# Performance work log

Hardware: AMD Instinct MI355X
Metric: run time of the kernel (lower is better)

The kernel has to match this reference:

```python
import jax, jax.numpy as jnp
import numpy as np

EPS = 1e-10

def norm_t(x, axis):
    # zero-mean + L2 normalize along `axis` (standard NCC normalization)
    xc = x - jnp.mean(x, axis=axis, keepdims=True)
    return xc / (jnp.linalg.norm(xc, axis=axis, keepdims=True) + EPS)

def setup_inputs() -> dict:
    key = jax.random.key(0)
    k1, k2 = jax.random.split(key)
    input_compressed = jax.random.normal(k1, (1, 16, 131072), dtype=jnp.float32)  # [B, K, N]
    cmat = jax.random.normal(k2, (16, 1024), dtype=jnp.float32)                   # [K, D]
    return {"input_compressed": input_compressed, "cmat": cmat}

def reference(input_compressed, cmat):
    a = norm_t(input_compressed, axis=-2)          # [B, K, N], normalized over K
    b = norm_t(cmat, axis=0)                       # [K, D],    normalized over K
    ncc = jnp.einsum('bkn,kd->bnd', a, b)          # [B, N, D] correlation volume
    # torch: argmax(transpose(ncc,-2,-1), dim=-2) -> argmax over D -> [B, N]
    pred_depths = jnp.argmax(ncc, axis=-1)         # [B, N] int depth-bin indices
    return pred_depths
```

## Files before the change

### kernel.cpp

```cpp
#include <hip/hip_runtime.h>
#include <hip/hip_bf16.h>
#include <math.h>

#define N_PTS  131072
#define K_DIM  16
#define D_BINS 1024
#define MARGIN_P 6e-4f

typedef short bf16x8 __attribute__((ext_vector_type(8)));
typedef float f32x4  __attribute__((ext_vector_type(4)));

#define WS_OFF_BN  64
#define WS_OFF_B1  65600
#define WS_OFF_B2  98368
#define WS_OFF_WL  131152
#define WS_NEED    655440

__device__ __forceinline__ void norm_np(const float* __restrict__ p,
                                        int stride, int n, float* __restrict__ a) {
#pragma clang fp contract(off)
    float v[K_DIM];
#pragma unroll
    for (int k = 0; k < K_DIM; ++k) v[k] = p[(size_t)k * stride + n];
    float s = v[0];
#pragma unroll
    for (int k = 1; k < K_DIM; ++k) s = s + v[k];
    const float mean = s / 16.0f;
    float sq[K_DIM];
#pragma unroll
    for (int k = 0; k < K_DIM; ++k) { a[k] = v[k] - mean; sq[k] = a[k] * a[k]; }
    float ss = sq[0];
#pragma unroll
    for (int k = 1; k < K_DIM; ++k) ss = ss + sq[k];
    const float denom = sqrtf(ss) + 1e-10f;
#pragma unroll
    for (int k = 0; k < K_DIM; ++k) a[k] = a[k] / denom;
}

__device__ __forceinline__ unsigned short bf16_bits(float f) {
    __hip_bfloat16 h = __float2bfloat16(f);
    unsigned short u;
    __builtin_memcpy(&u, &h, 2);
    return u;
}
__device__ __forceinline__ float bf16_val(float f) {
    return __bfloat162float(__float2bfloat16(f));
}

__device__ __forceinline__ unsigned v_med3u(unsigned a, unsigned b, unsigned c) {
    unsigned d;
    asm("v_med3_u32 %0, %1, %2, %3" : "=v"(d) : "v"(a), "v"(b), "v"(c));
    return d;
}

__global__ __launch_bounds__(256) void prep_b(
    const float* __restrict__ cmat, float* __restrict__ bnT,
    unsigned short* __restrict__ B1, unsigned short* __restrict__ B2,
    int* __restrict__ wl_count) {
#pragma clang fp contract(off)
    if (blockIdx.x == 0 && threadIdx.x == 0) *wl_count = 0;
    const int d = blockIdx.x * 256 + threadIdx.x;
    if (d >= D_BINS) return;

    float t[K_DIM];
    norm_np(cmat, D_BINS, d, t);

    const int tile = d >> 4, n = d & 15;
#pragma unroll
    for (int k = 0; k < K_DIM; ++k) {
        bnT[d * K_DIM + k] = t[k];
        const float hi_f = bf16_val(t[k]);
        const int idx = tile * 256 + ((k >> 3) * 16 + n) * 8 + (k & 7);
        B1[idx] = bf16_bits(t[k]);
        B2[idx] = bf16_bits(t[k] - hi_f);
    }
}

__global__ __launch_bounds__(512, 4) void mfma_screen(
    const float* __restrict__ x, const uint4* __restrict__ Bfrag,
    int* __restrict__ out, int* __restrict__ wl, int* __restrict__ wl_count) {
#pragma clang fp contract(off)
    __shared__ uint4 ldsB[4096];

    {
#pragma unroll
        for (int j = 0; j < 8; ++j)
            ldsB[threadIdx.x + j * 512] = Bfrag[threadIdx.x + j * 512];
    }

    const int lane = threadIdx.x & 63;
    const int wv   = threadIdx.x >> 6;
    const int W    = blockIdx.x * 8 + wv;
    const int P    = W * 16;
    const int m    = lane & 15;
    const int q    = lane >> 4;

    bf16x8 A, A2;
    {
        float a[K_DIM];
        norm_np(x, N_PTS, P + m, a);
        unsigned short els[8];
#pragma unroll
        for (int j = 0; j < 8; ++j) {
            const int k = (q & 1) * 8 + j;
            if (q < 2) els[j] = bf16_bits(a[k]);
            else       els[j] = bf16_bits(a[k] - bf16_val(a[k]));
        }
        __builtin_memcpy(&A, els, 16);
        A2 = (q < 2) ? A : (bf16x8)(short)0;
    }

    __syncthreads();

    const uint4* b1p = ldsB + (lane & 31);
    const uint4* b2p = ldsB + 2048 + (lane & 31);

    unsigned ub1[4], ub2[4];
#pragma unroll
    for (int r = 0; r < 4; ++r) { ub1[r] = 0u; ub2[r] = 0u; }

    const unsigned mask  = 0xFFFFF800u;
    const unsigned dbase = 2047u - (unsigned)m;

#pragma unroll 4
    for (int i = 0; i < 64; ++i) {
        const uint4 w1 = b1p[i * 32];
        const uint4 w2 = b2p[i * 32];
        const bf16x8 bf1 = __builtin_bit_cast(bf16x8, w1);
        const bf16x8 bf2 = __builtin_bit_cast(bf16x8, w2);

        f32x4 acc = __builtin_amdgcn_mfma_f32_16x16x32_bf16(
            A, bf1, (f32x4){2.f, 2.f, 2.f, 2.f}, 0, 0, 0);
        acc = __builtin_amdgcn_mfma_f32_16x16x32_bf16(A2, bf2, acc, 0, 0, 0);

        const unsigned dcomp = dbase - (unsigned)(i * 16);
#pragma unroll
        for (int r = 0; r < 4; ++r) {
            const unsigned u   = (__float_as_uint(acc[r]) & mask) | dcomp;
            const unsigned nb2 = v_med3u(ub1[r], ub2[r], u);
            ub1[r] = max(ub1[r], u);
            ub2[r] = nb2;
        }
    }

#pragma unroll
    for (int r = 0; r < 4; ++r) {
        unsigned u1 = ub1[r], u2 = ub2[r];
#pragma unroll
        for (int s = 1; s <= 8; s <<= 1) {
            const unsigned o1 = (unsigned)__shfl_xor((int)u1, s, 16);
            const unsigned o2 = (unsigned)__shfl_xor((int)u2, s, 16);
            const unsigned n1 = max(u1, o1);
            u2 = max(min(u1, o1), max(u2, o2));
            u1 = n1;
        }
        if (m == 0) {
            const int p  = P + q * 4 + r;
            const float s1 = __uint_as_float(u1 & mask);
            const float s2 = __uint_as_float(u2 & mask);
            if (s1 - s2 > MARGIN_P) {
                out[p] = 2047 - (int)(u1 & 2047u);
            } else {
                const int pos = atomicAdd(wl_count, 1);
                wl[pos] = p;
            }
        }
    }
}

__global__ __launch_bounds__(256) void ncc_exact_refine(
    const float* __restrict__ x, const float* __restrict__ bnT,
    int* __restrict__ out, const int* __restrict__ wl,
    const int* __restrict__ wl_count) {
#pragma clang fp contract(off)
    const int count  = *wl_count;
    const int lane   = threadIdx.x & 63;
    const int wave   = (blockIdx.x * 256 + threadIdx.x) >> 6;
    const int nwaves = (gridDim.x * 256) >> 6;

    for (int i = wave; i < count; i += nwaves) {
        const int n = wl[i];
        float a[K_DIM];
        norm_np(x, N_PTS, n, a);

        float best = -3.402823466e38f;
        int   idx  = 0x7fffffff;
        const float4* b4 = (const float4*)bnT;
        for (int t = 0; t < 16; ++t) {
            const int d = t * 64 + lane;
            const float4 q0 = b4[d * 4 + 0];
            const float4 q1 = b4[d * 4 + 1];
            const float4 q2 = b4[d * 4 + 2];
            const float4 q3 = b4[d * 4 + 3];
            float sc;
            sc = a[0] * q0.x;
            sc = sc + a[1]  * q0.y; sc = sc + a[2]  * q0.z; sc = sc + a[3]  * q0.w;
            sc = sc + a[4]  * q1.x; sc = sc + a[5]  * q1.y; sc = sc + a[6]  * q1.z;
            sc = sc + a[7]  * q1.w; sc = sc + a[8]  * q2.x; sc = sc + a[9]  * q2.y;
            sc = sc + a[10] * q2.z; sc = sc + a[11] * q2.w; sc = sc + a[12] * q3.x;
            sc = sc + a[13] * q3.y; sc = sc + a[14] * q3.z; sc = sc + a[15] * q3.w;
            if (sc > best) { best = sc; idx = d; }
        }
#pragma unroll
        for (int mk = 1; mk <= 32; mk <<= 1) {
            const float ob = __shfl_xor(best, mk);
            const int   oi = __shfl_xor(idx,  mk);
            if (ob > best || (ob == best && oi < idx)) { best = ob; idx = oi; }
        }
        if (lane == 0) out[n] = idx;
    }
}

__global__ __launch_bounds__(256) void ncc_argmax_np32(
    const float* __restrict__ x, const float* __restrict__ bnT,
    int* __restrict__ out) {
#pragma clang fp contract(off)
    const int n = blockIdx.x * 256 + threadIdx.x;
    float a[K_DIM];
    norm_np(x, N_PTS, n, a);

    float best = -3.402823466e38f;
    int   idx  = 0;
    const float4* b4 = (const float4*)bnT;
#pragma unroll 2
    for (int d = 0; d < D_BINS; ++d) {
        const float4 q0 = b4[d * 4 + 0];
        const float4 q1 = b4[d * 4 + 1];
        const float4 q2 = b4[d * 4 + 2];
        const float4 q3 = b4[d * 4 + 3];
        float sc;
        sc = a[0] * q0.x;
        sc = sc + a[1]  * q0.y; sc = sc + a[2]  * q0.z; sc = sc + a[3]  * q0.w;
        sc = sc + a[4]  * q1.x; sc = sc + a[5]  * q1.y; sc = sc + a[6]  * q1.z;
        sc = sc + a[7]  * q1.w; sc = sc + a[8]  * q2.x; sc = sc + a[9]  * q2.y;
        sc = sc + a[10] * q2.z; sc = sc + a[11] * q2.w; sc = sc + a[12] * q3.x;
        sc = sc + a[13] * q3.y; sc = sc + a[14] * q3.z; sc = sc + a[15] * q3.w;
        if (sc > best) { best = sc; idx = d; }
    }
    out[n] = idx;
}

__global__ __launch_bounds__(256) void normalize_rows_only(
    const float* __restrict__ cmat, float* __restrict__ bnT) {
#pragma clang fp contract(off)
    const int d = blockIdx.x * 256 + threadIdx.x;
    if (d >= D_BINS) return;
    float t[K_DIM];
    norm_np(cmat, D_BINS, d, t);
#pragma unroll
    for (int k = 0; k < K_DIM; ++k) bnT[d * K_DIM + k] = t[k];
}

extern "C" void kernel_launch(void* const* d_in, const int* in_sizes, int n_in,
                              void* d_out, int out_size, void* d_ws, size_t ws_size,
                              hipStream_t stream) {
    const float* x    = (const float*)d_in[0];
    const float* cmat = (const float*)d_in[1];
    int* out = (int*)d_out;
    char* ws = (char*)d_ws;

    if (ws_size >= (size_t)WS_NEED) {
        int*            wl_count = (int*)ws;
        float*          bnT      = (float*)(ws + WS_OFF_BN);
        unsigned short* B1       = (unsigned short*)(ws + WS_OFF_B1);
        unsigned short* B2       = (unsigned short*)(ws + WS_OFF_B2);
        int*            wl       = (int*)(ws + WS_OFF_WL);

        prep_b<<<4, 256, 0, stream>>>(cmat, bnT, B1, B2, wl_count);
        mfma_screen<<<1024, 512, 0, stream>>>(
            x, (const uint4*)(ws + WS_OFF_B1), out, wl, wl_count);
        ncc_exact_refine<<<512, 256, 0, stream>>>(x, bnT, out, wl, wl_count);
    } else {
        float* bnT = (float*)(ws + WS_OFF_BN);
        normalize_rows_only<<<4, 256, 0, stream>>>(cmat, bnT);
        ncc_argmax_np32<<<512, 256, 0, stream>>>(x, bnT, out);
    }
}
```

Measured before the change: 103.9 us.

## Switch screening MFMA to 32x32x16 tiles with three-term split-bf16 product

The screening kernel now uses 32x32x16 bf16 MFMA so each wave processes 32 points against 32 depth bins per step, and the B fragment layout in prep_b is rebuilt to match. The split-precision product changes from two half-empty 16x16 MFMAs (with a zeroed A2 half) to three full MFMAs (hi*hi, lo*hi, hi*lo), which drops the zero-padding waste. The grid is halved to match 32 points per wave. Each thread now holds 16 accumulators plus 32 running top-2 registers, which raises register pressure and may lower occupancy.

```diff
diff --git a/kernel.cpp b/kernel.cpp
--- a/kernel.cpp
+++ b/kernel.cpp
@@ -9,6 +9,7 @@
 
 typedef short bf16x8 __attribute__((ext_vector_type(8)));
 typedef float f32x4  __attribute__((ext_vector_type(4)));
+typedef float f32x16 __attribute__((ext_vector_type(16)));
 
 #define WS_OFF_BN  64
 #define WS_OFF_B1  65600
@@ -65,12 +66,12 @@
     float t[K_DIM];
     norm_np(cmat, D_BINS, d, t);
 
-    const int tile = d >> 4, n = d & 15;
+    const int tile = d >> 5, col = d & 31;
 #pragma unroll
     for (int k = 0; k < K_DIM; ++k) {
         bnT[d * K_DIM + k] = t[k];
         const float hi_f = bf16_val(t[k]);
-        const int idx = tile * 256 + ((k >> 3) * 16 + n) * 8 + (k & 7);
+        const int idx = tile * 512 + (k >> 3) * 256 + col * 8 + (k & 7);
         B1[idx] = bf16_bits(t[k]);
         B2[idx] = bf16_bits(t[k] - hi_f);
     }
@@ -91,51 +92,55 @@
     const int lane = threadIdx.x & 63;
     const int wv   = threadIdx.x >> 6;
     const int W    = blockIdx.x * 8 + wv;
-    const int P    = W * 16;
-    const int m    = lane & 15;
-    const int q    = lane >> 4;
-
-    bf16x8 A, A2;
+    const int P    = W * 32;
+    const int col  = lane & 31;
+    const int kh   = (lane >> 5) << 3;
+
+    bf16x8 Ahi, Alo;
     {
         float a[K_DIM];
-        norm_np(x, N_PTS, P + m, a);
-        unsigned short els[8];
+        norm_np(x, N_PTS, P + col, a);
+        unsigned short h[8], l[8];
 #pragma unroll
         for (int j = 0; j < 8; ++j) {
-            const int k = (q & 1) * 8 + j;
-            if (q < 2) els[j] = bf16_bits(a[k]);
-            else       els[j] = bf16_bits(a[k] - bf16_val(a[k]));
-        }
-        __builtin_memcpy(&A, els, 16);
-        A2 = (q < 2) ? A : (bf16x8)(short)0;
+            const float v = a[kh + j];
+            h[j] = bf16_bits(v);
+            l[j] = bf16_bits(v - bf16_val(v));
+        }
+        __builtin_memcpy(&Ahi, h, 16);
+        __builtin_memcpy(&Alo, l, 16);
     }
 
     __syncthreads();
 
-    const uint4* b1p = ldsB + (lane & 31);
-    const uint4* b2p = ldsB + 2048 + (lane & 31);
-
-    unsigned ub1[4], ub2[4];
-#pragma unroll
-    for (int r = 0; r < 4; ++r) { ub1[r] = 0u; ub2[r] = 0u; }
+    const uint4* b1p = ldsB + lane;
+    const uint4* b2p = ldsB + 2048 + lane;
+
+    f32x16 cb;
+#pragma unroll
+    for (int r = 0; r < 16; ++r) cb[r] = 2.0f;
+
+    unsigned ub1[16], ub2[16];
+#pragma unroll
+    for (int r = 0; r < 16; ++r) { ub1[r] = 0u; ub2[r] = 0u; }
 
     const unsigned mask  = 0xFFFFF800u;
-    const unsigned dbase = 2047u - (unsigned)m;
+    const unsigned dbase = 2047u - (unsigned)col;
 
 #pragma unroll 4
-    for (int i = 0; i < 64; ++i) {
-        const uint4 w1 = b1p[i * 32];
-        const uint4 w2 = b2p[i * 32];
+    for (int t = 0; t < 32; ++t) {
+        const uint4 w1 = b1p[t * 64];
+        const uint4 w2 = b2p[t * 64];
         const bf16x8 bf1 = __builtin_bit_cast(bf16x8, w1);
         const bf16x8 bf2 = __builtin_bit_cast(bf16x8, w2);
 
-        f32x4 acc = __builtin_amdgcn_mfma_f32_16x16x32_bf16(
-            A, bf1, (f32x4){2.f, 2.f, 2.f, 2.f}, 0, 0, 0);
-        acc = __builtin_amdgcn_mfma_f32_16x16x32_bf16(A2, bf2, acc, 0, 0, 0);
-
-        const unsigned dcomp = dbase - (unsigned)(i * 16);
-#pragma unroll
-        for (int r = 0; r < 4; ++r) {
+        f32x16 acc = __builtin_amdgcn_mfma_f32_32x32x16_bf16(Ahi, bf1, cb, 0, 0, 0);
+        acc = __builtin_amdgcn_mfma_f32_32x32x16_bf16(Alo, bf1, acc, 0, 0, 0);
+        acc = __builtin_amdgcn_mfma_f32_32x32x16_bf16(Ahi, bf2, acc, 0, 0, 0);
+
+        const unsigned dcomp = dbase - (unsigned)(t * 32);
+#pragma unroll
+        for (int r = 0; r < 16; ++r) {
             const unsigned u   = (__float_as_uint(acc[r]) & mask) | dcomp;
             const unsigned nb2 = v_med3u(ub1[r], ub2[r], u);
             ub1[r] = max(ub1[r], u);
@@ -144,18 +149,18 @@
     }
 
 #pragma unroll
-    for (int r = 0; r < 4; ++r) {
+    for (int r = 0; r < 16; ++r) {
         unsigned u1 = ub1[r], u2 = ub2[r];
 #pragma unroll
-        for (int s = 1; s <= 8; s <<= 1) {
-            const unsigned o1 = (unsigned)__shfl_xor((int)u1, s, 16);
-            const unsigned o2 = (unsigned)__shfl_xor((int)u2, s, 16);
+        for (int s = 1; s <= 16; s <<= 1) {
+            const unsigned o1 = (unsigned)__shfl_xor((int)u1, s, 32);
+            const unsigned o2 = (unsigned)__shfl_xor((int)u2, s, 32);
             const unsigned n1 = max(u1, o1);
             u2 = max(min(u1, o1), max(u2, o2));
             u1 = n1;
         }
-        if (m == 0) {
-            const int p  = P + q * 4 + r;
+        if (col == 0) {
+            const int p  = P + (r & 3) + 8 * (r >> 2) + 4 * (lane >> 5);
             const float s1 = __uint_as_float(u1 & mask);
             const float s2 = __uint_as_float(u2 & mask);
             if (s1 - s2 > MARGIN_P) {
@@ -267,7 +272,7 @@
         int*            wl       = (int*)(ws + WS_OFF_WL);
 
         prep_b<<<4, 256, 0, stream>>>(cmat, bnT, B1, B2, wl_count);
-        mfma_screen<<<1024, 512, 0, stream>>>(
+        mfma_screen<<<512, 512, 0, stream>>>(
             x, (const uint4*)(ws + WS_OFF_B1), out, wl, wl_count);
         ncc_exact_refine<<<512, 256, 0, stream>>>(x, bnT, out, wl, wl_count);
     } else {
```

New measurement: 106.5 us. 2.5% more time.

## Fuse exact refinement into MFMA screen kernel, drop global worklist and atomics

Applied to the files above, without the earlier changes.

Ambiguous points whose top-two margin is too small are no longer pushed to a global worklist with atomics for a third kernel. Each wave now collects its failing points into a ballot-built bitmask and refines them exactly in place against the fp32 normalized table. This removes one kernel launch, the atomic counter, and the worklist traffic. The cost is load imbalance, since waves that happen to hold many ambiguous points stall their block while the rest finish.

```diff
diff --git a/kernel.cpp b/kernel.cpp
--- a/kernel.cpp
+++ b/kernel.cpp
@@ -13,8 +13,7 @@
 #define WS_OFF_BN  64
 #define WS_OFF_B1  65600
 #define WS_OFF_B2  98368
-#define WS_OFF_WL  131152
-#define WS_NEED    655440
+#define WS_NEED    131136
 
 __device__ __forceinline__ void norm_np(const float* __restrict__ p,
                                         int stride, int n, float* __restrict__ a) {
@@ -55,10 +54,8 @@
 
 __global__ __launch_bounds__(256) void prep_b(
     const float* __restrict__ cmat, float* __restrict__ bnT,
-    unsigned short* __restrict__ B1, unsigned short* __restrict__ B2,
-    int* __restrict__ wl_count) {
-#pragma clang fp contract(off)
-    if (blockIdx.x == 0 && threadIdx.x == 0) *wl_count = 0;
+    unsigned short* __restrict__ B1, unsigned short* __restrict__ B2) {
+#pragma clang fp contract(off)
     const int d = blockIdx.x * 256 + threadIdx.x;
     if (d >= D_BINS) return;
 
@@ -78,7 +75,7 @@
 
 __global__ __launch_bounds__(512, 4) void mfma_screen(
     const float* __restrict__ x, const uint4* __restrict__ Bfrag,
-    int* __restrict__ out, int* __restrict__ wl, int* __restrict__ wl_count) {
+    const float* __restrict__ bnT, int* __restrict__ out) {
 #pragma clang fp contract(off)
     __shared__ uint4 ldsB[4096];
 
@@ -143,6 +140,7 @@
         }
     }
 
+    unsigned fail16 = 0;
 #pragma unroll
     for (int r = 0; r < 4; ++r) {
         unsigned u1 = ub1[r], u2 = ub2[r];
@@ -154,34 +152,28 @@
             u2 = max(min(u1, o1), max(u2, o2));
             u1 = n1;
         }
+        int fail = 0;
         if (m == 0) {
             const int p  = P + q * 4 + r;
             const float s1 = __uint_as_float(u1 & mask);
             const float s2 = __uint_as_float(u2 & mask);
-            if (s1 - s2 > MARGIN_P) {
-                out[p] = 2047 - (int)(u1 & 2047u);
-            } else {
-                const int pos = atomicAdd(wl_count, 1);
-                wl[pos] = p;
-            }
-        }
-    }
-}
-
-__global__ __launch_bounds__(256) void ncc_exact_refine(
-    const float* __restrict__ x, const float* __restrict__ bnT,
-    int* __restrict__ out, const int* __restrict__ wl,
-    const int* __restrict__ wl_count) {
-#pragma clang fp contract(off)
-    const int count  = *wl_count;
-    const int lane   = threadIdx.x & 63;
-    const int wave   = (blockIdx.x * 256 + threadIdx.x) >> 6;
-    const int nwaves = (gridDim.x * 256) >> 6;
-
-    for (int i = wave; i < count; i += nwaves) {
-        const int n = wl[i];
+            if (s1 - s2 > MARGIN_P) out[p] = 2047 - (int)(u1 & 2047u);
+            else fail = 1;
+        }
+        const unsigned long long bm = __ballot(fail);
+        fail16 |= (unsigned)((bm      ) & 1ull) << (r);
+        fail16 |= (unsigned)((bm >> 16) & 1ull) << (4 + r);
+        fail16 |= (unsigned)((bm >> 32) & 1ull) << (8 + r);
+        fail16 |= (unsigned)((bm >> 48) & 1ull) << (12 + r);
+    }
+
+    while (fail16) {
+        const int s = __builtin_ffs((int)fail16) - 1;
+        fail16 &= fail16 - 1;
+        const int p = P + s;
+
         float a[K_DIM];
-        norm_np(x, N_PTS, n, a);
+        norm_np(x, N_PTS, p, a);
 
         float best = -3.402823466e38f;
         int   idx  = 0x7fffffff;
@@ -207,7 +199,7 @@
             const int   oi = __shfl_xor(idx,  mk);
             if (ob > best || (ob == best && oi < idx)) { best = ob; idx = oi; }
         }
-        if (lane == 0) out[n] = idx;
+        if (lane == 0) out[p] = idx;
     }
 }
 
@@ -260,16 +252,13 @@
     char* ws = (char*)d_ws;
 
     if (ws_size >= (size_t)WS_NEED) {
-        int*            wl_count = (int*)ws;
-        float*          bnT      = (float*)(ws + WS_OFF_BN);
-        unsigned short* B1       = (unsigned short*)(ws + WS_OFF_B1);
-        unsigned short* B2       = (unsigned short*)(ws + WS_OFF_B2);
-        int*            wl       = (int*)(ws + WS_OFF_WL);
-
-        prep_b<<<4, 256, 0, stream>>>(cmat, bnT, B1, B2, wl_count);
+        float*          bnT = (float*)(ws + WS_OFF_BN);
+        unsigned short* B1  = (unsigned short*)(ws + WS_OFF_B1);
+        unsigned short* B2  = (unsigned short*)(ws + WS_OFF_B2);
+
+        prep_b<<<4, 256, 0, stream>>>(cmat, bnT, B1, B2);
         mfma_screen<<<1024, 512, 0, stream>>>(
-            x, (const uint4*)(ws + WS_OFF_B1), out, wl, wl_count);
-        ncc_exact_refine<<<512, 256, 0, stream>>>(x, bnT, out, wl, wl_count);
+            x, (const uint4*)(ws + WS_OFF_B1), bnT, out);
     } else {
         float* bnT = (float*)(ws + WS_OFF_BN);
         normalize_rows_only<<<4, 256, 0, stream>>>(cmat, bnT);
```

After: 104.6 us. About the same (+0.7%).
